# Performance work log

Hardware: AMD Instinct MI355X
Metric: run time of the kernel (lower is better)

Reference implementation:

```python
import jax, jax.numpy as jnp
import numpy as np

B, N, C, H, W, NH, SR = 16, 4096, 128, 64, 64, 4, 8
LN_EPS = 1e-5


def _conv(x, w, b, stride, padding, groups=1):
    y = jax.lax.conv_general_dilated(
        x, w, (stride, stride), padding,
        feature_group_count=groups,
        dimension_numbers=('NCHW', 'OIHW', 'NCHW'))
    return y + b[None, :, None, None]


def _layernorm(x, g, b):
    m = jnp.mean(x, axis=-1, keepdims=True)
    v = jnp.mean((x - m) ** 2, axis=-1, keepdims=True)
    return (x - m) / jnp.sqrt(v + LN_EPS) * g + b


def setup_inputs() -> dict:
    key = jax.random.key(0)
    ks = jax.random.split(key, 12)
    s = 0.02
    return {
        'x': jax.random.normal(ks[0], (B, N, C), jnp.float32),
        'q_w': jax.random.normal(ks[1], (C, C), jnp.float32) * s,
        'sr1_w': jax.random.normal(ks[2], (C, C, SR, SR), jnp.float32) * s,
        'sr1_b': jnp.zeros((C,), jnp.float32),
        'n1_g': jnp.ones((C,), jnp.float32),
        'n1_b': jnp.zeros((C,), jnp.float32),
        'sr2_w': jax.random.normal(ks[3], (C, C, SR // 2, SR // 2), jnp.float32) * s,
        'sr2_b': jnp.zeros((C,), jnp.float32),
        'n2_g': jnp.ones((C,), jnp.float32),
        'n2_b': jnp.zeros((C,), jnp.float32),
        'kv1_w': jax.random.normal(ks[4], (C, C), jnp.float32) * s,
        'kv2_w': jax.random.normal(ks[5], (C, C), jnp.float32) * s,
        'lc1_w': jax.random.normal(ks[6], (C // 2, 1, 3, 3), jnp.float32) * s,
        'lc1_b': jnp.zeros((C // 2,), jnp.float32),
        'lc2_w': jax.random.normal(ks[7], (C // 2, 1, 3, 3), jnp.float32) * s,
        'lc2_b': jnp.zeros((C // 2,), jnp.float32),
        'proj_w': jax.random.normal(ks[8], (C, C), jnp.float32) * s,
        'proj_b': jnp.zeros((C,), jnp.float32),
        'h': H,
        'w': W,
    }


def _forward(x, q_w, sr1_w, sr1_b, n1_g, n1_b, sr2_w, sr2_b, n2_g, n2_b,
             kv1_w, kv2_w, lc1_w, lc1_b, lc2_w, lc2_b, proj_w, proj_b, h, w):
    b, n, c = x.shape
    nh, sr = NH, SR
    hh = nh // 2          # heads per branch
    d = c // nh           # head dim
    scale = d ** -0.5

    q = (x @ q_w.T).reshape(b, n, nh, d).transpose(0, 2, 1, 3)  # (b,nh,n,d)
    x_img = x.transpose(0, 2, 1).reshape(b, c, h, w)

    def branch(sr_w, sr_b, g, beta, kv_w, lc_w, lc_b, stride, q_part):
        hp, wp = h // stride, w // stride
        m = hp * wp
        t = _conv(x_img, sr_w, sr_b, stride, 'VALID')          # (b,c,hp,wp)
        t = t.reshape(b, c, m).transpose(0, 2, 1)              # (b,m,c)
        t = jax.nn.gelu(_layernorm(t, g, beta), approximate=False)
        kv = (t @ kv_w.T).reshape(b, m, 2, hh, d).transpose(2, 0, 3, 1, 4)
        k, v = kv[0], kv[1]                                    # (b,hh,m,d)
        attn = jax.nn.softmax(
            jnp.einsum('bhnd,bhmd->bhnm', q_part, k) * scale, axis=-1)
        # local depthwise conv on v over the reduced spatial grid
        v_img = v.transpose(0, 2, 1, 3).reshape(b, m, c // 2)
        v_img = v_img.transpose(0, 2, 1).reshape(b, c // 2, hp, wp)
        v_loc = _conv(v_img, lc_w, lc_b, 1, [(1, 1), (1, 1)], groups=c // 2)
        v = v + v_loc.reshape(b, hh, d, m).transpose(0, 1, 3, 2)
        out = jnp.einsum('bhnm,bhmd->bhnd', attn, v)           # (b,hh,n,d)
        return out.transpose(0, 2, 1, 3).reshape(b, n, c // 2)

    x1 = branch(sr1_w, sr1_b, n1_g, n1_b, kv1_w, lc1_w, lc1_b, sr, q[:, :hh])
    x2 = branch(sr2_w, sr2_b, n2_g, n2_b, kv2_w, lc2_w, lc2_b, sr // 2, q[:, hh:])
    return jnp.concatenate([x1, x2], axis=-1) @ proj_w.T + proj_b


def reference(x, q_w, sr1_w, sr1_b, n1_g, n1_b, sr2_w, sr2_b, n2_g, n2_b,
              kv1_w, kv2_w, lc1_w, lc1_b, lc2_w, lc2_b, proj_w, proj_b, h, w):
    return _forward(x, q_w, sr1_w, sr1_b, n1_g, n1_b, sr2_w, sr2_b, n2_g, n2_b,
                    kv1_w, kv2_w, lc1_w, lc1_b, lc2_w, lc2_b, proj_w, proj_b, h, w)
```

## Files before the change

kernel.cpp:

```cpp
#include <hip/hip_runtime.h>
#include <math.h>

#define B_ 16
#define N_ 4096

typedef __attribute__((ext_vector_type(8))) short short8v;
typedef __attribute__((ext_vector_type(4))) short short4v;
typedef __attribute__((ext_vector_type(4))) float f32x4;

__device__ __forceinline__ unsigned short f2bf(float f) {
  unsigned int u = __float_as_uint(f);
  return (unsigned short)((u + 0x7FFFu + ((u >> 16) & 1u)) >> 16);
}

__device__ __forceinline__ unsigned int pk2(float a, float b) {
  return (unsigned int)f2bf(a) | ((unsigned int)f2bf(b) << 16);
}

__device__ __forceinline__ short8v cvt8f(const float* p) {
  float4 a = *reinterpret_cast<const float4*>(p);
  float4 b = *reinterpret_cast<const float4*>(p + 4);
  short8v r;
  r[0] = (short)f2bf(a.x); r[1] = (short)f2bf(a.y);
  r[2] = (short)f2bf(a.z); r[3] = (short)f2bf(a.w);
  r[4] = (short)f2bf(b.x); r[5] = (short)f2bf(b.y);
  r[6] = (short)f2bf(b.z); r[7] = (short)f2bf(b.w);
  return r;
}

__global__ __launch_bounds__(256) void prep(const float* __restrict__ x,
    unsigned short* __restrict__ xT, unsigned short* __restrict__ xb,
    const float* __restrict__ a, const float* __restrict__ b,
    const float* __restrict__ c, const float* __restrict__ d,
    const float* __restrict__ s1, const float* __restrict__ s2,
    unsigned short* __restrict__ wa, unsigned short* __restrict__ wb,
    unsigned short* __restrict__ wc, unsigned short* __restrict__ wd,
    unsigned short* __restrict__ w1, unsigned short* __restrict__ w2) {
  __shared__ float lds[32 * 132];
  const int t = threadIdx.x;
  if (blockIdx.x < 2048) {
    const int bb = blockIdx.x >> 7, pt = blockIdx.x & 127;
    const int ptile = pt * 32;
    for (int i = t; i < 1024; i += 256) {
      int p = i >> 5, c4 = (i & 31) << 2;
      *reinterpret_cast<float4*>(&lds[p * 132 + c4]) =
          *reinterpret_cast<const float4*>(
              x + ((size_t)(bb * 4096 + ptile + p)) * 128 + c4);
    }
    __syncthreads();
    for (int i = t; i < 1024; i += 256) {
      int p = i >> 5, c4 = (i & 31) << 2;
      const float* s = &lds[p * 132 + c4];
      uint2 u;
      u.x = pk2(s[0], s[1]);
      u.y = pk2(s[2], s[3]);
      *reinterpret_cast<uint2*>(
          xb + ((size_t)(bb * 4096 + ptile + p)) * 128 + c4) = u;
    }
    const int ch = t >> 1, p0 = (t & 1) * 16;
    unsigned short* dst = xT + (size_t)bb * 524288 + ch * 4096 + ptile + p0;
    uint4 u0, u1;
    u0.x = pk2(lds[(p0 + 0) * 132 + ch], lds[(p0 + 1) * 132 + ch]);
    u0.y = pk2(lds[(p0 + 2) * 132 + ch], lds[(p0 + 3) * 132 + ch]);
    u0.z = pk2(lds[(p0 + 4) * 132 + ch], lds[(p0 + 5) * 132 + ch]);
    u0.w = pk2(lds[(p0 + 6) * 132 + ch], lds[(p0 + 7) * 132 + ch]);
    u1.x = pk2(lds[(p0 + 8) * 132 + ch], lds[(p0 + 9) * 132 + ch]);
    u1.y = pk2(lds[(p0 + 10) * 132 + ch], lds[(p0 + 11) * 132 + ch]);
    u1.z = pk2(lds[(p0 + 12) * 132 + ch], lds[(p0 + 13) * 132 + ch]);
    u1.w = pk2(lds[(p0 + 14) * 132 + ch], lds[(p0 + 15) * 132 + ch]);
    *reinterpret_cast<uint4*>(dst) = u0;
    *reinterpret_cast<uint4*>(dst + 8) = u1;
  } else {
    int i = (blockIdx.x - 2048) * 256 + t;
    if (i < 16384) wa[i] = f2bf(a[i]);
    else if (i < 32768) { int o = i - 16384; wb[o] = f2bf(b[o]); }
    else if (i < 49152) { int o = i - 32768; wc[o] = f2bf(c[o]); }
    else if (i < 65536) { int o = i - 49152; wd[o] = f2bf(d[o]); }
    else if (i < 65536 + 1048576) { int o = i - 65536; w1[o] = f2bf(s1[o]); }
    else { int o = i - 65536 - 1048576; w2[o] = f2bf(s2[o]); }
  }
}

template <int SRV, int KSP>
__device__ void conv_body(int bx, int by, const unsigned short* __restrict__ xT,
    const unsigned short* __restrict__ W, float* __restrict__ part) {
  constexpr int WP = 64 / SRV;
  constexpr int M = WP * WP;
  constexpr int ROWS = B_ * M;
  constexpr int SS = SRV * SRV;
  constexpr int KTOT = 128 * SS;
  constexpr int LSS = (SRV == 8) ? 6 : 4;
  constexpr int LM = (SRV == 8) ? 6 : 8;
  constexpr int LWP = (SRV == 8) ? 3 : 4;
  const int t = threadIdx.x;
  const int wid = t >> 6, lane = t & 63;
  const int lrow = lane & 15, lk = (lane >> 4) << 3;
  const int r0 = bx * 128 + wid * 32;
  const int kb0 = by * KSP;
  int rbase[2], pixoff[2];
#pragma unroll
  for (int m = 0; m < 2; m++) {
    int row = r0 + m * 16 + lrow;
    int b = row >> LM, p = row & (M - 1);
    int ph = p >> LWP, pw = p & (WP - 1);
    rbase[m] = b << 19;
    pixoff[m] = (ph * SRV) * 64 + pw * SRV;
  }
  f32x4 acc[2][8];
#pragma unroll
  for (int m = 0; m < 2; m++)
#pragma unroll
    for (int n = 0; n < 8; n++) acc[m][n] = (f32x4)(0.f);
  for (int k0 = 0; k0 < KSP; k0 += 32) {
    int k = kb0 + k0 + lk;
    int ci = k >> LSS;
    int rem = k & (SS - 1);
    short8v a[2], bf[8];
#pragma unroll
    for (int m = 0; m < 2; m++) {
      if constexpr (SRV == 8) {
        a[m] = *reinterpret_cast<const short8v*>(
            xT + (size_t)rbase[m] + ci * 4096 + pixoff[m] + (rem >> 3) * 64);
      } else {
        int kh0 = rem >> 2;
        short4v lo = *reinterpret_cast<const short4v*>(
            xT + (size_t)rbase[m] + ci * 4096 + pixoff[m] + kh0 * 64);
        short4v hi = *reinterpret_cast<const short4v*>(
            xT + (size_t)rbase[m] + ci * 4096 + pixoff[m] + (kh0 + 1) * 64);
        short8v av;
        av[0] = lo[0]; av[1] = lo[1]; av[2] = lo[2]; av[3] = lo[3];
        av[4] = hi[0]; av[5] = hi[1]; av[6] = hi[2]; av[7] = hi[3];
        a[m] = av;
      }
    }
#pragma unroll
    for (int n = 0; n < 8; n++)
      bf[n] = *reinterpret_cast<const short8v*>(
          W + (size_t)(n * 16 + lrow) * KTOT + k);
#pragma unroll
    for (int m = 0; m < 2; m++)
#pragma unroll
      for (int n = 0; n < 8; n++)
        acc[m][n] = __builtin_amdgcn_mfma_f32_16x16x32_bf16(a[m], bf[n],
                                                            acc[m][n], 0, 0, 0);
  }
  const int rr = (lane >> 4) << 2;
#pragma unroll
  for (int m = 0; m < 2; m++)
#pragma unroll
    for (int n = 0; n < 8; n++) {
      int cc = n * 16 + lrow;
#pragma unroll
      for (int j = 0; j < 4; j++)
        part[((size_t)by * ROWS + r0 + m * 16 + rr + j) * 128 + cc] =
            acc[m][n][j];
    }
}

template <bool A_BF16, bool OUT_BF16, bool HAS_BIAS>
__device__ void gemm_body(int bx, const void* __restrict__ Araw,
    const unsigned short* __restrict__ W, const float* __restrict__ bias,
    void* __restrict__ out) {
  const int t = threadIdx.x;
  const int wid = t >> 6, lane = t & 63;
  const int lrow = lane & 15, lk = (lane >> 4) << 3;
  const int r0 = bx * 128 + wid * 32;
  f32x4 acc[2][8];
#pragma unroll
  for (int m = 0; m < 2; m++)
#pragma unroll
    for (int n = 0; n < 8; n++) acc[m][n] = (f32x4)(0.f);
#pragma unroll
  for (int k0 = 0; k0 < 128; k0 += 32) {
    short8v a[2], bf[8];
#pragma unroll
    for (int m = 0; m < 2; m++) {
      if constexpr (A_BF16)
        a[m] = *reinterpret_cast<const short8v*>(
            (const unsigned short*)Araw + (size_t)(r0 + m * 16 + lrow) * 128 +
            k0 + lk);
      else
        a[m] = cvt8f((const float*)Araw + (size_t)(r0 + m * 16 + lrow) * 128 +
                     k0 + lk);
    }
#pragma unroll
    for (int n = 0; n < 8; n++)
      bf[n] = *reinterpret_cast<const short8v*>(
          W + (size_t)(n * 16 + lrow) * 128 + k0 + lk);
#pragma unroll
    for (int m = 0; m < 2; m++)
#pragma unroll
      for (int n = 0; n < 8; n++)
        acc[m][n] = __builtin_amdgcn_mfma_f32_16x16x32_bf16(a[m], bf[n],
                                                            acc[m][n], 0, 0, 0);
  }
  const int rr = (lane >> 4) << 2;
#pragma unroll
  for (int m = 0; m < 2; m++)
#pragma unroll
    for (int n = 0; n < 8; n++) {
      int cc = n * 16 + lrow;
      float bv = HAS_BIAS ? bias[cc] : 0.f;
#pragma unroll
      for (int j = 0; j < 4; j++) {
        size_t idx = (size_t)(r0 + m * 16 + rr + j) * 128 + cc;
        float v = acc[m][n][j] + bv;
        if constexpr (OUT_BF16)
          ((unsigned short*)out)[idx] = f2bf(v);
        else
          ((float*)out)[idx] = v;
      }
    }
}

__global__ __launch_bounds__(256) void conv_q(
    const unsigned short* __restrict__ xT, const unsigned short* __restrict__ w1b,
    const unsigned short* __restrict__ w2b, float* __restrict__ part1,
    float* __restrict__ part2, unsigned short* __restrict__ xb,
    const unsigned short* __restrict__ wq) {
  const int bid = blockIdx.x;
  if (bid < 128) {
    conv_body<8, 512>(bid & 7, bid >> 3, xT, w1b, part1);
  } else if (bid < 256) {
    int j = bid - 128;
    conv_body<4, 512>(j & 31, j >> 5, xT, w2b, part2);
  } else {
    gemm_body<true, true, false>(bid - 256, xb, wq, nullptr, xb);
  }
}

__global__ __launch_bounds__(128) void ln_all(const float* __restrict__ part1,
    const float* __restrict__ part2, const float* __restrict__ cb1,
    const float* __restrict__ g1, const float* __restrict__ be1,
    const float* __restrict__ cb2, const float* __restrict__ g2,
    const float* __restrict__ be2, unsigned short* __restrict__ out1,
    unsigned short* __restrict__ out2) {
  const int t = threadIdx.x;
  int row = blockIdx.x;
  const float* part; const float *cb, *g, *be; unsigned short* out;
  int nsplit, rows;
  if (row < 1024) {
    part = part1; cb = cb1; g = g1; be = be1; out = out1;
    nsplit = 16; rows = 1024;
  } else {
    row -= 1024;
    part = part2; cb = cb2; g = g2; be = be2; out = out2;
    nsplit = 4; rows = 4096;
  }
  float v = cb[t];
  for (int s = 0; s < nsplit; s++)
    v += part[((size_t)s * rows + row) * 128 + t];
  float sv = v, sq = v * v;
#pragma unroll
  for (int off = 32; off > 0; off >>= 1) {
    sv += __shfl_down(sv, off, 64);
    sq += __shfl_down(sq, off, 64);
  }
  __shared__ float red0[2], red1[2];
  if ((t & 63) == 0) {
    red0[t >> 6] = sv;
    red1[t >> 6] = sq;
  }
  __syncthreads();
  float mean = (red0[0] + red0[1]) * (1.f / 128.f);
  float var = (red1[0] + red1[1]) * (1.f / 128.f) - mean * mean;
  float y = (v - mean) * rsqrtf(var + 1e-5f) * g[t] + be[t];
  out[(size_t)row * 128 + t] = f2bf(y * 0.5f * (1.f + erff(y * 0.70710678118f)));
}

__device__ void kv_body(int bx, const unsigned short* __restrict__ A,
    const unsigned short* __restrict__ W, unsigned short* __restrict__ kb,
    float* __restrict__ vr) {
  const int t = threadIdx.x;
  const int wid = t >> 6, lane = t & 63;
  const int lrow = lane & 15, lk = (lane >> 4) << 3;
  const int r0 = bx * 128 + wid * 32;
  f32x4 acc[2][8];
#pragma unroll
  for (int m = 0; m < 2; m++)
#pragma unroll
    for (int n = 0; n < 8; n++) acc[m][n] = (f32x4)(0.f);
#pragma unroll
  for (int k0 = 0; k0 < 128; k0 += 32) {
    short8v a[2], bf[8];
#pragma unroll
    for (int m = 0; m < 2; m++)
      a[m] = *reinterpret_cast<const short8v*>(
          A + (size_t)(r0 + m * 16 + lrow) * 128 + k0 + lk);
#pragma unroll
    for (int n = 0; n < 8; n++)
      bf[n] = *reinterpret_cast<const short8v*>(
          W + (size_t)(n * 16 + lrow) * 128 + k0 + lk);
#pragma unroll
    for (int m = 0; m < 2; m++)
#pragma unroll
      for (int n = 0; n < 8; n++)
        acc[m][n] = __builtin_amdgcn_mfma_f32_16x16x32_bf16(a[m], bf[n],
                                                            acc[m][n], 0, 0, 0);
  }
  const int rr = (lane >> 4) << 2;
#pragma unroll
  for (int m = 0; m < 2; m++)
#pragma unroll
    for (int n = 0; n < 8; n++) {
      int cc = n * 16 + lrow;
#pragma unroll
      for (int j = 0; j < 4; j++) {
        int r = r0 + m * 16 + rr + j;
        float v = acc[m][n][j];
        if (cc < 64)
          kb[(size_t)r * 64 + cc] = f2bf(v);
        else
          vr[(size_t)r * 64 + (cc - 64)] = v;
      }
    }
}

__global__ __launch_bounds__(256) void kv_all(
    const unsigned short* __restrict__ t1b, const unsigned short* __restrict__ wkv1,
    unsigned short* __restrict__ kb1, float* __restrict__ vr1,
    const unsigned short* __restrict__ t2b, const unsigned short* __restrict__ wkv2,
    unsigned short* __restrict__ kb2, float* __restrict__ vr2) {
  if (blockIdx.x < 8)
    kv_body(blockIdx.x, t1b, wkv1, kb1, vr1);
  else
    kv_body(blockIdx.x - 8, t2b, wkv2, kb2, vr2);
}

template <int WP>
__device__ void dw_body(int idx, const float* __restrict__ vr,
    const float* __restrict__ lw, const float* __restrict__ lb,
    float* __restrict__ vp) {
  constexpr int M = WP * WP;
  constexpr int LM = (WP == 8) ? 6 : 8;
  constexpr int LWPc = (WP == 8) ? 3 : 4;
  int ch = idx & 63;
  int rest = idx >> 6;
  int m = rest & (M - 1);
  int bb = rest >> LM;
  int y = m >> LWPc, x0 = m & (WP - 1);
  float s = lb[ch];
#pragma unroll
  for (int ky = 0; ky < 3; ky++) {
    int yy = y + ky - 1;
    if (yy < 0 || yy >= WP) continue;
#pragma unroll
    for (int kx = 0; kx < 3; kx++) {
      int xx = x0 + kx - 1;
      if (xx < 0 || xx >= WP) continue;
      s += vr[((size_t)(bb * M + yy * WP + xx)) * 64 + ch] *
           lw[ch * 9 + ky * 3 + kx];
    }
  }
  vp[idx] = vr[((size_t)(bb * M + m)) * 64 + ch] + s;
}

__global__ __launch_bounds__(256) void dw_all(const float* __restrict__ vr1,
    const float* __restrict__ lw1, const float* __restrict__ lb1,
    float* __restrict__ v1p, const float* __restrict__ vr2,
    const float* __restrict__ lw2, const float* __restrict__ lb2,
    float* __restrict__ v2p) {
  if (blockIdx.x < 256)
    dw_body<8>(blockIdx.x * 256 + threadIdx.x, vr1, lw1, lb1, v1p);
  else
    dw_body<16>((blockIdx.x - 256) * 256 + threadIdx.x, vr2, lw2, lb2, v2p);
}

template <int M>
__device__ void tv_body(int blk, const float* __restrict__ vp,
    unsigned short* __restrict__ vT, float* lds) {
  constexpr int TPB = M / 32;
  const int t = threadIdx.x;
  const int b = blk / TPB, mt = blk % TPB;
  const int m0 = mt * 32;
  for (int i = t; i < 512; i += 256) {
    int m = i >> 4, c4 = (i & 15) << 2;
    *reinterpret_cast<float4*>(&lds[m * 68 + c4]) =
        *reinterpret_cast<const float4*>(vp + ((size_t)(b * M + m0 + m)) * 64 + c4);
  }
  __syncthreads();
  const int c = t >> 2, ms = (t & 3) * 8;
  unsigned short* dst = vT + ((size_t)b * 64 + c) * M + m0 + ms;
  uint4 u;
  u.x = pk2(lds[(ms + 0) * 68 + c], lds[(ms + 1) * 68 + c]);
  u.y = pk2(lds[(ms + 2) * 68 + c], lds[(ms + 3) * 68 + c]);
  u.z = pk2(lds[(ms + 4) * 68 + c], lds[(ms + 5) * 68 + c]);
  u.w = pk2(lds[(ms + 6) * 68 + c], lds[(ms + 7) * 68 + c]);
  *reinterpret_cast<uint4*>(dst) = u;
}

__global__ __launch_bounds__(256) void tv_all(const float* __restrict__ v1p,
    unsigned short* __restrict__ vT1, const float* __restrict__ v2p,
    unsigned short* __restrict__ vT2) {
  __shared__ float lds[32 * 68];
  if (blockIdx.x < 32)
    tv_body<64>(blockIdx.x, v1p, vT1, lds);
  else
    tv_body<256>(blockIdx.x - 32, v2p, vT2, lds);
}

template <int M, int QOFF, bool K_LDS>
__device__ void attn_head(int b, int q0, int h,
    const unsigned short* __restrict__ qb, const unsigned short* Ks,
    const unsigned short* __restrict__ kbg, const unsigned short* __restrict__ vT,
    unsigned short* __restrict__ xc, unsigned short* Plw) {
  constexpr int HM = (M > 64) ? 64 : M;
  constexpr int NCH = M / HM;
  constexpr int PSTR = HM + 8;
  constexpr int MT = M / 16;
  constexpr int HKS = HM / 32;
  const int lane = threadIdx.x & 63;
  const int lrow = lane & 15, g = lane >> 4;
  const int lk = g * 8;
  const size_t bm = (size_t)b * M;
  const size_t qrow = ((size_t)b * 4096 + q0 + lrow) * 128;
  const int qoff = QOFF + h * 32;
  const float scale = 0.17677669529663687f;
  short8v qf = *reinterpret_cast<const short8v*>(qb + qrow + qoff + lk);
  f32x4 s[MT];
#pragma unroll
  for (int mt = 0; mt < MT; mt++) {
    short8v kf;
    if constexpr (K_LDS)
      kf = *reinterpret_cast<const short8v*>(
          Ks + (mt * 16 + lrow) * 72 + h * 32 + lk);
    else
      kf = *reinterpret_cast<const short8v*>(
          kbg + (bm + mt * 16 + lrow) * 64 + h * 32 + lk);
    s[mt] =
        __builtin_amdgcn_mfma_f32_16x16x32_bf16(kf, qf, (f32x4)(0.f), 0, 0, 0);
  }
  float l = 0.f;
#pragma unroll
  for (int mt = 0; mt < MT; mt++)
#pragma unroll
    for (int j = 0; j < 4; j++) {
      float p = __expf(s[mt][j] * scale);
      s[mt][j] = p;
      l += p;
    }
  l += __shfl_xor(l, 16, 64);
  l += __shfl_xor(l, 32, 64);
  f32x4 o[2];
  o[0] = (f32x4)(0.f);
  o[1] = (f32x4)(0.f);
#pragma unroll
  for (int half = 0; half < NCH; half++) {
#pragma unroll
    for (int mt2 = 0; mt2 < HM / 16; mt2++) {
      int mt = half * (HM / 16) + mt2;
      uint2 pw;
      pw.x = pk2(s[mt][0], s[mt][1]);
      pw.y = pk2(s[mt][2], s[mt][3]);
      *reinterpret_cast<uint2*>(&Plw[lrow * PSTR + mt2 * 16 + 4 * g]) = pw;
    }
    f32x4 oh[2];
    oh[0] = (f32x4)(0.f);
    oh[1] = (f32x4)(0.f);
#pragma unroll
    for (int ks = 0; ks < HKS; ks++) {
      short8v pf = *reinterpret_cast<const short8v*>(
          &Plw[lrow * PSTR + ks * 32 + lk]);
#pragma unroll
      for (int dt = 0; dt < 2; dt++) {
        short8v vf = *reinterpret_cast<const short8v*>(
            vT + ((size_t)b * 64 + h * 32 + dt * 16 + lrow) * M + half * HM +
            ks * 32 + lk);
        oh[dt] =
            __builtin_amdgcn_mfma_f32_16x16x32_bf16(vf, pf, oh[dt], 0, 0, 0);
      }
    }
#pragma unroll
    for (int dt = 0; dt < 2; dt++) o[dt] += oh[dt];
  }
  float linv = 1.f / l;
  unsigned short* orow = xc + qrow + qoff;
#pragma unroll
  for (int dt = 0; dt < 2; dt++) {
    uint2 u;
    u.x = pk2(o[dt][0] * linv, o[dt][1] * linv);
    u.y = pk2(o[dt][2] * linv, o[dt][3] * linv);
    *reinterpret_cast<uint2*>(orow + dt * 16 + 4 * g) = u;
  }
}

__global__ __launch_bounds__(256) void attn_all(
    const unsigned short* __restrict__ qb, const unsigned short* __restrict__ kb1,
    const unsigned short* __restrict__ vT1, const unsigned short* __restrict__ kb2,
    const unsigned short* __restrict__ vT2, unsigned short* __restrict__ xc) {
  __shared__ unsigned short Ks2[256 * 72];
  __shared__ unsigned short Pl[4 * 16 * 72];
  const int t = threadIdx.x;
  const int b = blockIdx.x >> 6, qt = blockIdx.x & 63;
  for (int i = t; i < 2048; i += 256) {
    int row = i >> 3, seg = i & 7;
    *reinterpret_cast<uint4*>(&Ks2[row * 72 + seg * 8]) =
        *reinterpret_cast<const uint4*>(kb2 + ((size_t)b * 256 + row) * 64 +
                                        seg * 8);
  }
  __syncthreads();
  const int wid = t >> 6;
  unsigned short* Plw = Pl + wid * 16 * 72;
  const int q0 = qt * 64 + wid * 16;
  attn_head<256, 64, true>(b, q0, 0, qb, Ks2, nullptr, vT2, xc, Plw);
  attn_head<256, 64, true>(b, q0, 1, qb, Ks2, nullptr, vT2, xc, Plw);
  attn_head<64, 0, false>(b, q0, 0, qb, nullptr, kb1, vT1, xc, Plw);
  attn_head<64, 0, false>(b, q0, 1, qb, nullptr, kb1, vT1, xc, Plw);
}

__global__ __launch_bounds__(256) void proj(const unsigned short* __restrict__ A,
    const unsigned short* __restrict__ W, const float* __restrict__ bias,
    float* __restrict__ out) {
  gemm_body<true, false, true>(blockIdx.x, A, W, bias, out);
}

extern "C" void kernel_launch(void* const* d_in, const int* in_sizes, int n_in,
                              void* d_out, int out_size, void* d_ws,
                              size_t ws_size, hipStream_t stream) {
  (void)in_sizes; (void)n_in; (void)out_size; (void)ws_size;
  const float* x      = (const float*)d_in[0];
  const float* q_w    = (const float*)d_in[1];
  const float* sr1_w  = (const float*)d_in[2];
  const float* sr1_b  = (const float*)d_in[3];
  const float* n1_g   = (const float*)d_in[4];
  const float* n1_b   = (const float*)d_in[5];
  const float* sr2_w  = (const float*)d_in[6];
  const float* sr2_b  = (const float*)d_in[7];
  const float* n2_g   = (const float*)d_in[8];
  const float* n2_b   = (const float*)d_in[9];
  const float* kv1_w  = (const float*)d_in[10];
  const float* kv2_w  = (const float*)d_in[11];
  const float* lc1_w  = (const float*)d_in[12];
  const float* lc1_b  = (const float*)d_in[13];
  const float* lc2_w  = (const float*)d_in[14];
  const float* lc2_b  = (const float*)d_in[15];
  const float* proj_w = (const float*)d_in[16];
  const float* proj_b = (const float*)d_in[17];

  char* w = (char*)d_ws;
  unsigned short* wq    = (unsigned short*)(w);
  unsigned short* wkv1  = (unsigned short*)(w + 32768);
  unsigned short* wkv2  = (unsigned short*)(w + 65536);
  unsigned short* wproj = (unsigned short*)(w + 98304);
  unsigned short* w1b   = (unsigned short*)(w + 131072);
  unsigned short* w2b   = (unsigned short*)(w + 2228224);
  unsigned short* xT  = (unsigned short*)(w + 2752512);
  unsigned short* kb1 = (unsigned short*)(w + 19529728);
  unsigned short* kb2 = (unsigned short*)(w + 19660800);
  float* part1 = (float*)(w + 33685504);
  float* part2 = (float*)(w + 42074112);
  unsigned short* xcb = (unsigned short*)(w + 33685504);
  unsigned short* xb  = (unsigned short*)(w + 50462720);
  unsigned short* qb  = xb;
  unsigned short* t1b = (unsigned short*)(w + 69468160);
  unsigned short* t2b = (unsigned short*)(w + 69730304);
  float* vr1 = (float*)(w + 70778880);
  float* vr2 = (float*)(w + 71041024);
  float* v1p = (float*)(w + 72089600);
  float* v2p = (float*)(w + 72351744);
  unsigned short* vT1 = (unsigned short*)(w + 73400320);
  unsigned short* vT2 = (unsigned short*)(w + 73531392);

  prep<<<7424, 256, 0, stream>>>(x, xT, xb, q_w, kv1_w, kv2_w, proj_w, sr1_w,
                                 sr2_w, wq, wkv1, wkv2, wproj, w1b, w2b);
  conv_q<<<768, 256, 0, stream>>>(xT, w1b, w2b, part1, part2, xb, wq);
  ln_all<<<5120, 128, 0, stream>>>(part1, part2, sr1_b, n1_g, n1_b, sr2_b, n2_g,
                                   n2_b, t1b, t2b);
  kv_all<<<40, 256, 0, stream>>>(t1b, wkv1, kb1, vr1, t2b, wkv2, kb2, vr2);
  dw_all<<<1280, 256, 0, stream>>>(vr1, lc1_w, lc1_b, v1p, vr2, lc2_w, lc2_b, v2p);
  tv_all<<<160, 256, 0, stream>>>(v1p, vT1, v2p, vT2);
  attn_all<<<1024, 256, 0, stream>>>(qb, kb1, vT1, kb2, vT2, xcb);
  proj<<<512, 256, 0, stream>>>(xcb, wproj, proj_b, (float*)d_out);
}
```

Before: 118.7 us.

## Fuse output projection into attention kernel via per-wave LDS staging

Each wave writes its 16x128 attention output tile to shared memory instead of global memory, then runs the projection GEMM with MFMA against wproj and writes the fp32 result plus bias directly. This removes the separate proj launch and the global round trip of the bf16 intermediate. In exchange it adds about 17KB of extra LDS per block, which may lower occupancy. wproj is now read from global or L2 by every wave, and the output stores use a strided, less coalesced pattern.

```diff
diff --git a/kernel.cpp b/kernel.cpp
--- a/kernel.cpp
+++ b/kernel.cpp
@@ -403,7 +403,7 @@
 __device__ void attn_head(int b, int q0, int h,
     const unsigned short* __restrict__ qb, const unsigned short* Ks,
     const unsigned short* __restrict__ kbg, const unsigned short* __restrict__ vT,
-    unsigned short* __restrict__ xc, unsigned short* Plw) {
+    unsigned short* Pow, unsigned short* Plw) {
   constexpr int HM = (M > 64) ? 64 : M;
   constexpr int NCH = M / HM;
   constexpr int PSTR = HM + 8;
@@ -474,22 +474,24 @@
     for (int dt = 0; dt < 2; dt++) o[dt] += oh[dt];
   }
   float linv = 1.f / l;
-  unsigned short* orow = xc + qrow + qoff;
 #pragma unroll
   for (int dt = 0; dt < 2; dt++) {
     uint2 u;
     u.x = pk2(o[dt][0] * linv, o[dt][1] * linv);
     u.y = pk2(o[dt][2] * linv, o[dt][3] * linv);
-    *reinterpret_cast<uint2*>(orow + dt * 16 + 4 * g) = u;
+    *reinterpret_cast<uint2*>(&Pow[lrow * 136 + qoff + dt * 16 + 4 * g]) = u;
   }
 }
 
 __global__ __launch_bounds__(256) void attn_all(
     const unsigned short* __restrict__ qb, const unsigned short* __restrict__ kb1,
     const unsigned short* __restrict__ vT1, const unsigned short* __restrict__ kb2,
-    const unsigned short* __restrict__ vT2, unsigned short* __restrict__ xc) {
+    const unsigned short* __restrict__ vT2,
+    const unsigned short* __restrict__ wproj, const float* __restrict__ pb,
+    float* __restrict__ out) {
   __shared__ unsigned short Ks2[256 * 72];
   __shared__ unsigned short Pl[4 * 16 * 72];
+  __shared__ unsigned short Po[4 * 16 * 136];
   const int t = threadIdx.x;
   const int b = blockIdx.x >> 6, qt = blockIdx.x & 63;
   for (int i = t; i < 2048; i += 256) {
@@ -499,19 +501,41 @@
                                         seg * 8);
   }
   __syncthreads();
-  const int wid = t >> 6;
+  const int wid = t >> 6, lane = t & 63;
+  const int lrow = lane & 15, g = lane >> 4;
+  const int lk = g * 8;
   unsigned short* Plw = Pl + wid * 16 * 72;
+  unsigned short* Pow = Po + wid * 16 * 136;
   const int q0 = qt * 64 + wid * 16;
-  attn_head<256, 64, true>(b, q0, 0, qb, Ks2, nullptr, vT2, xc, Plw);
-  attn_head<256, 64, true>(b, q0, 1, qb, Ks2, nullptr, vT2, xc, Plw);
-  attn_head<64, 0, false>(b, q0, 0, qb, nullptr, kb1, vT1, xc, Plw);
-  attn_head<64, 0, false>(b, q0, 1, qb, nullptr, kb1, vT1, xc, Plw);
-}
-
-__global__ __launch_bounds__(256) void proj(const unsigned short* __restrict__ A,
-    const unsigned short* __restrict__ W, const float* __restrict__ bias,
-    float* __restrict__ out) {
-  gemm_body<true, false, true>(blockIdx.x, A, W, bias, out);
+  attn_head<256, 64, true>(b, q0, 0, qb, Ks2, nullptr, vT2, Pow, Plw);
+  attn_head<256, 64, true>(b, q0, 1, qb, Ks2, nullptr, vT2, Pow, Plw);
+  attn_head<64, 0, false>(b, q0, 0, qb, nullptr, kb1, vT1, Pow, Plw);
+  attn_head<64, 0, false>(b, q0, 1, qb, nullptr, kb1, vT1, Pow, Plw);
+  f32x4 pacc[8];
+#pragma unroll
+  for (int n = 0; n < 8; n++) pacc[n] = (f32x4)(0.f);
+#pragma unroll
+  for (int k0 = 0; k0 < 128; k0 += 32) {
+    short8v a = *reinterpret_cast<const short8v*>(&Pow[lrow * 136 + k0 + lk]);
+    short8v bf[8];
+#pragma unroll
+    for (int n = 0; n < 8; n++)
+      bf[n] = *reinterpret_cast<const short8v*>(
+          wproj + (size_t)(n * 16 + lrow) * 128 + k0 + lk);
+#pragma unroll
+    for (int n = 0; n < 8; n++)
+      pacc[n] = __builtin_amdgcn_mfma_f32_16x16x32_bf16(a, bf[n], pacc[n],
+                                                        0, 0, 0);
+  }
+  const int rr = g * 4;
+#pragma unroll
+  for (int n = 0; n < 8; n++) {
+    int cc = n * 16 + lrow;
+    float bv = pb[cc];
+#pragma unroll
+    for (int j = 0; j < 4; j++)
+      out[(size_t)(b * 4096 + q0 + rr + j) * 128 + cc] = pacc[n][j] + bv;
+  }
 }
 
 extern "C" void kernel_launch(void* const* d_in, const int* in_sizes, int n_in,
@@ -549,7 +573,6 @@
   unsigned short* kb2 = (unsigned short*)(w + 19660800);
   float* part1 = (float*)(w + 33685504);
   float* part2 = (float*)(w + 42074112);
-  unsigned short* xcb = (unsigned short*)(w + 33685504);
   unsigned short* xb  = (unsigned short*)(w + 50462720);
   unsigned short* qb  = xb;
   unsigned short* t1b = (unsigned short*)(w + 69468160);
@@ -569,6 +592,6 @@
   kv_all<<<40, 256, 0, stream>>>(t1b, wkv1, kb1, vr1, t2b, wkv2, kb2, vr2);
   dw_all<<<1280, 256, 0, stream>>>(vr1, lc1_w, lc1_b, v1p, vr2, lc2_w, lc2_b, v2p);
   tv_all<<<160, 256, 0, stream>>>(v1p, vT1, v2p, vT2);
-  attn_all<<<1024, 256, 0, stream>>>(qb, kb1, vT1, kb2, vT2, xcb);
-  proj<<<512, 256, 0, stream>>>(xcb, wproj, proj_b, (float*)d_out);
-}
+  attn_all<<<1024, 256, 0, stream>>>(qb, kb1, vT1, kb2, vT2, wproj, proj_b,
+                                     (float*)d_out);
+}
```

Result: no change. 116.9 us, median of 2 (-1.6%).
